# Kernel optimization log

Measured on AMD Instinct MI355X. Metric: run time of the kernel, lower is better.

## Reference

```python
import jax, jax.numpy as jnp
import numpy as np

MASK_RATIO = 0.75
B, N, D = 32, 1024, 768


def setup_inputs() -> dict:
    key = jax.random.key(0)
    k1, k2, k3 = jax.random.split(key, 3)
    return {
        "patch_embeddings": jax.random.normal(k1, (B, N, D), dtype=jnp.float32),
        "noise": jax.random.uniform(k2, (B, N), dtype=jnp.float32),
        "mask_emb": jax.random.normal(k3, (D,), dtype=jnp.float32) * 0.02,
    }


def reference(patch_embeddings, noise, mask_emb):
    b, n, d = patch_embeddings.shape
    k = int(MASK_RATIO * n)  # total_patches_to_mask (fixed per batch)

    # torch: perm = rand.argsort(dim=1); mask = base_mask.gather(1, perm)
    # => mask[b, j] = (perm[b, j] < k)
    perm = jnp.argsort(noise, axis=1)
    bool_mask = perm < k  # [B, N]

    # replace masked patches with the learned mask embedding
    with_mask = jnp.where(bool_mask[:, :, None], mask_emb[None, None, :], patch_embeddings)

    # torch.where over a bool mask returns SORTED indices; exploit the fixed
    # masked count: stable argsort of bool puts the (n-k) False indices first
    # (in ascending order) and the k True indices last (in ascending order).
    order = jnp.argsort(bool_mask, axis=1, stable=True)  # [B, N]
    unmasked_indices = order[:, : n - k]  # [B, N-k], sorted per row
    masked_indices = order[:, n - k :]    # [B, k],   sorted per row

    # batched compaction: gather the unmasked patches only
    unmasked_patches_only = jnp.take_along_axis(
        patch_embeddings, unmasked_indices[:, :, None], axis=1
    )  # [B, N-k, D]

    bool_mask_expanded = jnp.broadcast_to(bool_mask[:, :, None], (b, n, d))
    return (with_mask, unmasked_patches_only, bool_mask_expanded,
            masked_indices, unmasked_indices)
```

## Files before the change

### kernel.cpp

```cpp
#include <hip/hip_runtime.h>

#define B_  32
#define N_  1024
#define D_  768
#define K_  768
#define U_  256
#define D4_ 192

__global__ __launch_bounds__(128) void rank_scatter(const float* __restrict__ noise,
                                                    int* __restrict__ maskinfo) {
    const int b = blockIdx.x >> 3;
    const int i = ((blockIdx.x & 7) << 7) + threadIdx.x;
    const float* __restrict__ row = noise + b * N_;

    const unsigned int bi = __float_as_uint(row[i]);
    const unsigned long long ki = ((unsigned long long)bi << 10) | (unsigned int)i;

    int r = 0;
#pragma unroll 16
    for (int j = 0; j < N_; ++j) {
        const unsigned int bj = __float_as_uint(row[j]);
        const unsigned long long kj = ((unsigned long long)bj << 10) | (unsigned int)j;
        r += (kj < ki) ? 1 : 0;
    }
    maskinfo[b * N_ + r] = (i < K_) ? 1 : 0;
}

__global__ __launch_bounds__(1024) void index_lists(int* __restrict__ maskinfo,
                                                    float* __restrict__ masked_idx,
                                                    float* __restrict__ unmasked_idx) {
    const int b   = blockIdx.x;
    const int tid = threadIdx.x;
    const bool m  = maskinfo[b * N_ + tid] != 0;

    const unsigned long long bal = __ballot(m);
    const int lane = tid & 63;
    const int wave = tid >> 6;

    __shared__ int wsum[16];
    const int inwave = __popcll(bal & ((1ull << lane) - 1ull));
    if (lane == 0) wsum[wave] = __popcll(bal);
    __syncthreads();

    int off = 0;
    for (int w = 0; w < wave; ++w) off += wsum[w];
    const int p = off + inwave;

    if (m) {
        masked_idx[b * K_ + p] = (float)tid;
        maskinfo[b * N_ + tid] = -1;
    } else {
        const int u = tid - p;
        unmasked_idx[b * U_ + u] = (float)tid;
        maskinfo[b * N_ + tid] = u;
    }
}

#define ROWS_ 8
__global__ __launch_bounds__(192) void expand(const float4* __restrict__ patch,
                                              const float4* __restrict__ memb,
                                              const int* __restrict__ maskinfo,
                                              float4* __restrict__ with_mask,
                                              float4* __restrict__ unmasked_only,
                                              float4* __restrict__ bool_exp) {
    const int tid = threadIdx.x;
    const float4 me   = memb[tid];
    const float4 ONE  = make_float4(1.f, 1.f, 1.f, 1.f);
    const float4 ZERO = make_float4(0.f, 0.f, 0.f, 0.f);

    const int base = blockIdx.x * ROWS_;
#pragma unroll
    for (int it = 0; it < ROWS_; ++it) {
        const int rowi = base + it;
        const int info = maskinfo[rowi];
        const int o    = rowi * D4_ + tid;
        if (info < 0) {
            with_mask[o] = me;
            bool_exp[o]  = ONE;
        } else {
            const float4 p = patch[o];
            with_mask[o] = p;
            bool_exp[o]  = ZERO;
            const int b  = rowi >> 10;
            unmasked_only[(b * U_ + info) * D4_ + tid] = p;
        }
    }
}

extern "C" void kernel_launch(void* const* d_in, const int* in_sizes, int n_in,
                              void* d_out, int out_size, void* d_ws, size_t ws_size,
                              hipStream_t stream) {
    const float* patch = (const float*)d_in[0];
    const float* noise = (const float*)d_in[1];
    const float* memb  = (const float*)d_in[2];

    float* out  = (float*)d_out;
    float* out0 = out;
    float* out1 = out0 + (size_t)B_ * N_ * D_;
    float* out2 = out1 + (size_t)B_ * U_ * D_;
    float* out3 = out2 + (size_t)B_ * N_ * D_;
    float* out4 = out3 + (size_t)B_ * K_;

    int* maskinfo = (int*)d_ws;

    rank_scatter<<<B_ * 8, 128, 0, stream>>>(noise, maskinfo);
    index_lists<<<B_, 1024, 0, stream>>>(maskinfo, out3, out4);
    expand<<<(B_ * N_) / ROWS_, 192, 0, stream>>>(
        (const float4*)patch, (const float4*)memb, maskinfo,
        (float4*)out0, (float4*)out1, (float4*)out2);
}
```

Baseline: 343.0 us.

## Stage rank keys in LDS, use nontemporal stores, and double rows per block

The rank kernel now builds the 64-bit sort keys once into shared memory and compares against LDS instead of reloading and rebuilding each key from global memory in the inner loop. The expand kernel writes its large outputs with nontemporal stores to avoid polluting cache with streaming data. Rows per block in expand are doubled, which halves the grid size. The expand kernel is bandwidth bound and dominates the runtime, so the gains depend mostly on the nontemporal store behaviour.

```diff
diff --git a/kernel.cpp b/kernel.cpp
--- a/kernel.cpp
+++ b/kernel.cpp
@@ -7,22 +7,31 @@
 #define U_  256
 #define D4_ 192
 
+typedef float vfloat4 __attribute__((ext_vector_type(4)));
+
+__device__ __forceinline__ void nt_store4(float4* p, float4 v) {
+    vfloat4 nv = { v.x, v.y, v.z, v.w };
+    __builtin_nontemporal_store(nv, reinterpret_cast<vfloat4*>(p));
+}
+
 __global__ __launch_bounds__(128) void rank_scatter(const float* __restrict__ noise,
                                                     int* __restrict__ maskinfo) {
-    const int b = blockIdx.x >> 3;
-    const int i = ((blockIdx.x & 7) << 7) + threadIdx.x;
+    __shared__ unsigned long long keys[N_];
+    const int b    = blockIdx.x >> 3;
+    const int base = (blockIdx.x & 7) << 7;
     const float* __restrict__ row = noise + b * N_;
 
-    const unsigned int bi = __float_as_uint(row[i]);
-    const unsigned long long ki = ((unsigned long long)bi << 10) | (unsigned int)i;
+    for (int j = threadIdx.x; j < N_; j += 128)
+        keys[j] = ((unsigned long long)__float_as_uint(row[j]) << 10) | (unsigned)j;
+    __syncthreads();
 
+    const int i = base + threadIdx.x;
+    const unsigned long long ki = keys[i];
     int r = 0;
 #pragma unroll 16
-    for (int j = 0; j < N_; ++j) {
-        const unsigned int bj = __float_as_uint(row[j]);
-        const unsigned long long kj = ((unsigned long long)bj << 10) | (unsigned int)j;
-        r += (kj < ki) ? 1 : 0;
-    }
+    for (int j = 0; j < N_; ++j)
+        r += (keys[j] < ki) ? 1 : 0;
+
     maskinfo[b * N_ + r] = (i < K_) ? 1 : 0;
 }
 
@@ -56,7 +65,7 @@
     }
 }
 
-#define ROWS_ 8
+#define ROWS_ 16
 __global__ __launch_bounds__(192) void expand(const float4* __restrict__ patch,
                                               const float4* __restrict__ memb,
                                               const int* __restrict__ maskinfo,
@@ -75,14 +84,14 @@
         const int info = maskinfo[rowi];
         const int o    = rowi * D4_ + tid;
         if (info < 0) {
-            with_mask[o] = me;
-            bool_exp[o]  = ONE;
+            nt_store4(&with_mask[o], me);
+            nt_store4(&bool_exp[o],  ONE);
         } else {
             const float4 p = patch[o];
-            with_mask[o] = p;
-            bool_exp[o]  = ZERO;
-            const int b  = rowi >> 10;
-            unmasked_only[(b * U_ + info) * D4_ + tid] = p;
+            nt_store4(&with_mask[o], p);
+            nt_store4(&bool_exp[o],  ZERO);
+            const int b = rowi >> 10;
+            nt_store4(&unmasked_only[(b * U_ + info) * D4_ + tid], p);
         }
     }
 }
```

After: 310.4 us. 1.11x faster.
